# Optimization experiments

Measured on AMD Instinct MI355X. Metric: run time of the kernel, lower is better.

Reference implementation:

```python
import jax, jax.numpy as jnp
import numpy as np

N = 50000       # nodes
E = 800000      # edges (before self-loops)
G = 512         # graphs in batch
IN_DIM = 128
OUT_DIM = 8
DIMS = [(IN_DIM, 32), (32, 64), (64, 128), (128, 64)]
EPS = 1e-5


def setup_inputs() -> dict:
    key = jax.random.key(0)
    ks = jax.random.split(key, 40)
    def nrm(k, shape, s=0.05):
        return jax.random.normal(k, shape, jnp.float32) * s
    inp = {}
    inp["x"] = jax.random.normal(ks[0], (N, IN_DIM), jnp.float32)
    inp["edge_index"] = jax.random.randint(ks[1], (2, E), 0, N, dtype=jnp.int32)
    inp["batch"] = jnp.sort(jax.random.randint(ks[2], (N,), 0, G, dtype=jnp.int32))
    for i, (din, dout) in enumerate(DIMS, 1):
        inp[f"W{i}"]  = nrm(ks[3 * i + 0], (din, dout))
        inp[f"as{i}"] = nrm(ks[3 * i + 1], (dout,))
        inp[f"ad{i}"] = nrm(ks[3 * i + 2], (dout,))
        inp[f"b{i}"]  = jnp.zeros((dout,), jnp.float32)
        inp[f"g{i}"]  = jnp.ones((dout,), jnp.float32)   # BN gamma
        inp[f"be{i}"] = jnp.zeros((dout,), jnp.float32)  # BN beta
    inp["Wf"] = nrm(ks[20], (64, 32)); inp["bf"] = jnp.zeros((32,), jnp.float32)
    inp["Wc"] = nrm(ks[21], (32, OUT_DIM)); inp["bc"] = jnp.zeros((OUT_DIM,), jnp.float32)
    return inp


def gat_conv(x, src, dst, W, a_s, a_d, b):
    """PyG GATConv, heads=1: linear (no bias) -> per-edge attention with
    leaky_relu(0.2) -> segment softmax over incoming edges -> scatter-add -> bias."""
    h = x @ W                                   # [N, F]
    a_src = h @ a_s                             # [N]
    a_dst = h @ a_d                             # [N]
    e = jax.nn.leaky_relu(a_src[src] + a_dst[dst], 0.2)   # [E+N]
    m = jax.ops.segment_max(e, dst, num_segments=N)
    w = jnp.exp(e - m[dst])
    denom = jax.ops.segment_sum(w, dst, num_segments=N)
    alpha = w / denom[dst]                      # self-loops guarantee denom > 0
    out = jax.ops.segment_sum(alpha[:, None] * h[src], dst, num_segments=N)
    return out + b


def batch_norm(x, g, be):
    mu = x.mean(axis=0)
    var = x.var(axis=0)                         # biased, as torch training BN
    return (x - mu) * jax.lax.rsqrt(var + EPS) * g + be


def reference(x, edge_index, batch,
              W1, as1, ad1, b1, g1, be1,
              W2, as2, ad2, b2, g2, be2,
              W3, as3, ad3, b3, g3, be3,
              W4, as4, ad4, b4, g4, be4,
              Wf, bf, Wc, bc):
    loops = jnp.arange(N, dtype=edge_index.dtype)
    src = jnp.concatenate([edge_index[0], loops])   # GATConv adds self-loops
    dst = jnp.concatenate([edge_index[1], loops])
    params = [(W1, as1, ad1, b1, g1, be1), (W2, as2, ad2, b2, g2, be2),
              (W3, as3, ad3, b3, g3, be3), (W4, as4, ad4, b4, g4, be4)]
    h = x
    for (W, a_s, a_d, b, g, be) in params:
        h = jax.nn.leaky_relu(gat_conv(h, src, dst, W, a_s, a_d, b), 0.01)
        h = batch_norm(h, g, be)
    pooled = jax.ops.segment_sum(h, batch, num_segments=G)   # global_add_pool
    z = jax.nn.leaky_relu(pooled @ Wf + bf, 0.01)
    return jax.nn.sigmoid(z @ Wc + bc)
```

## Files before the change

### kernel.cpp

```cpp
#include <hip/hip_runtime.h>
#include <math.h>

constexpr int BLK = 256;
constexpr int NBLKA = 256;

static inline int cdiv(long a, long b) { return (int)((a + b - 1) / b); }

typedef __attribute__((ext_vector_type(8))) short short8;
typedef __attribute__((ext_vector_type(4))) float floatx4;

__device__ __forceinline__ unsigned short f2bf(float f) {
    unsigned u = __float_as_uint(f);
    unsigned r = u + 0x7fffu + ((u >> 16) & 1u);
    return (unsigned short)(r >> 16);
}
__device__ __forceinline__ float bf2f(unsigned short s) {
    return __uint_as_float(((unsigned)s) << 16);
}


__global__ void histA_k(const int* __restrict__ dst, int* __restrict__ histg,
                        int E, int nbkt, int chunk) {
    __shared__ int h[256];
    int tid = threadIdx.x, z = blockIdx.x;
    h[tid] = 0;
    __syncthreads();
    int e0 = z * chunk, e1 = min(E, e0 + chunk);
    for (int e = e0 + tid; e < e1; e += BLK) atomicAdd(&h[dst[e] >> 8], 1);
    __syncthreads();
    if (tid < nbkt) histg[z * nbkt + tid] = h[tid];
}

__global__ void bucket_scan_k(const int* __restrict__ histg, int* __restrict__ bucket_base,
                              int nbkt, int E, int* __restrict__ gs, int* __restrict__ ge,
                              int G, float* __restrict__ bnstats) {
    __shared__ int s[BLK];
    int t = threadIdx.x;
    int v = 0;
    if (t < nbkt)
        for (int z = 0; z < NBLKA; ++z) v += histg[z * nbkt + t];
    s[t] = v;
    __syncthreads();
    for (int o = 1; o < BLK; o <<= 1) {
        int tv = (t >= o) ? s[t - o] : 0;
        __syncthreads();
        s[t] += tv;
        __syncthreads();
    }
    if (t < nbkt) bucket_base[t] = s[t] - v;
    if (t == 0) bucket_base[nbkt] = E;
    for (int i = t; i < G; i += BLK) { gs[i] = 0x7fffffff; ge[i] = -1; }
    for (int i = t; i < 8192; i += BLK) bnstats[i] = 0.f;
}

__global__ void blk_scan_k(int* __restrict__ histg, const int* __restrict__ bucket_base,
                           int nbkt) {
    __shared__ int s[BLK];
    int t = threadIdx.x, b = blockIdx.x;
    int v = histg[t * nbkt + b];
    s[t] = v;
    __syncthreads();
    for (int o = 1; o < BLK; o <<= 1) {
        int tv = (t >= o) ? s[t - o] : 0;
        __syncthreads();
        s[t] += tv;
        __syncthreads();
    }
    histg[t * nbkt + b] = bucket_base[b] + s[t] - v;
}

__global__ void scatterA_k(const int* __restrict__ src, const int* __restrict__ dst,
                           const int* __restrict__ histg, unsigned* __restrict__ ebkt,
                           int E, int nbkt, int chunk) {
    __shared__ int cur[256];
    int tid = threadIdx.x, z = blockIdx.x;
    if (tid < nbkt) cur[tid] = histg[z * nbkt + tid];
    __syncthreads();
    int e0 = z * chunk, e1 = min(E, e0 + chunk);
    for (int e = e0 + tid; e < e1; e += BLK) {
        int d = dst[e];
        int b = d >> 8;
        int pos = atomicAdd(&cur[b], 1);
        ebkt[pos] = ((unsigned)(d & 255) << 16) | (unsigned)src[e];
    }
}

__global__ void csrB_k(const unsigned* __restrict__ ebkt, const int* __restrict__ bucket_base,
                       int* __restrict__ off, unsigned short* __restrict__ csr,
                       const int* __restrict__ batch, int* __restrict__ gs,
                       int* __restrict__ ge, int N, int E, int nbkt) {
    __shared__ int dg[256];
    __shared__ int sc[256];
    int t = threadIdx.x, b = blockIdx.x;
    int n0 = b << 8;
    int cnt = min(256, N - n0);
    dg[t] = (t < cnt) ? 1 : 0;
    __syncthreads();
    int e0 = bucket_base[b], e1 = bucket_base[b + 1];
    for (int e = e0 + t; e < e1; e += BLK) atomicAdd(&dg[ebkt[e] >> 16], 1);
    __syncthreads();
    int d = dg[t];
    sc[t] = d;
    __syncthreads();
    for (int o = 1; o < BLK; o <<= 1) {
        int tv = (t >= o) ? sc[t - o] : 0;
        __syncthreads();
        sc[t] += tv;
        __syncthreads();
    }
    int loff = sc[t] - d;
    int csrbase = e0 + n0;
    if (t < cnt) {
        off[n0 + t] = csrbase + loff;
        csr[csrbase + loff] = (unsigned short)(n0 + t);
        dg[t] = loff + 1;
    }
    if (b == nbkt - 1 && t == 0) off[N] = E + N;
    int n = n0 + t;
    if (n < N) {
        int bb = batch[n];
        if (n == 0) gs[bb] = 0;
        else {
            int pb = batch[n - 1];
            if (pb != bb) { gs[bb] = n; ge[pb] = n - 1; }
        }
        if (n == N - 1) ge[bb] = N - 1;
    }
    __syncthreads();
    for (int e = e0 + t; e < e1; e += BLK) {
        unsigned w = ebkt[e];
        int pos = atomicAdd(&dg[w >> 16], 1);
        csr[csrbase + pos] = (unsigned short)(w & 0xffff);
    }
}

template <int K, int NOUT, bool AFP32, bool HASBN>
__launch_bounds__(256)
__global__ void gemm_fused(const void* __restrict__ av, const float* __restrict__ W,
                           const float* __restrict__ a_s, const float* __restrict__ a_d,
                           const float* __restrict__ bnst, const float* __restrict__ g_prev,
                           const float* __restrict__ be_prev, float invN,
                           unsigned short* __restrict__ hb,
                           float* __restrict__ asrc, float* __restrict__ adst, int N) {
    constexpr int KF = K / 32;
    constexpr int NY = NOUT / 16;
    __shared__ float s_sca[K], s_scc[K], s_rs[K], s_rd[K], s_bd[2];
    int tid = threadIdx.x;
    if (tid < K) {
        float a = 1.f, c = 0.f;
        if (HASBN) {
            float su = 0.f, sq = 0.f;
#pragma unroll
            for (int s = 0; s < 8; ++s) {
                su += bnst[s * 256 + tid];
                sq += bnst[s * 256 + 128 + tid];
            }
            float mu = su * invN;
            float var = sq * invN - mu * mu;
            a = g_prev[tid] * rsqrtf(var + 1e-5f);
            c = be_prev[tid] - mu * a;
        }
        s_sca[tid] = a; s_scc[tid] = c;
    }
    __syncthreads();
    {
        if (tid < K) {
            const float* wr = W + (long)tid * NOUT;
            float rs = 0.f, rd = 0.f;
            for (int f = 0; f < NOUT; ++f) {
                float w = wr[f];
                rs += w * a_s[f];
                rd += w * a_d[f];
            }
            s_rs[tid] = rs; s_rd[tid] = rd;
        }
        __syncthreads();
        if (tid < 2) {
            const float* r = tid ? s_rd : s_rs;
            float b = 0.f;
            for (int k = 0; k < K; ++k) b += s_scc[k] * r[k];
            s_bd[tid] = b;
        }
        __syncthreads();
    }

    int wave = tid >> 6;
    int lane = tid & 63;
    int quad = lane >> 4;
    int r16 = lane & 15;
    int blockbase = blockIdx.x * 128;

    short8 afr[2][KF];
    bool valid[2];
#pragma unroll
    for (int rt = 0; rt < 2; ++rt) {
        int tilebase = blockbase + wave * 32 + rt * 16;
        valid[rt] = tilebase < N;
        if (!valid[rt]) continue;
        int arow = min(tilebase + r16, N - 1);
        if (AFP32) {
            const float* xr = (const float*)av + (long)arow * K;
#pragma unroll
            for (int kk = 0; kk < KF; ++kk) {
                float4 x0 = *(const float4*)(xr + kk * 32 + quad * 8);
                float4 x1 = *(const float4*)(xr + kk * 32 + quad * 8 + 4);
                short8 a;
                a[0] = (short)f2bf(x0.x); a[1] = (short)f2bf(x0.y);
                a[2] = (short)f2bf(x0.z); a[3] = (short)f2bf(x0.w);
                a[4] = (short)f2bf(x1.x); a[5] = (short)f2bf(x1.y);
                a[6] = (short)f2bf(x1.z); a[7] = (short)f2bf(x1.w);
                afr[rt][kk] = a;
            }
        } else {
            const unsigned short* hr = (const unsigned short*)av + (long)arow * K;
#pragma unroll
            for (int kk = 0; kk < KF; ++kk)
                afr[rt][kk] = *(const short8*)(hr + kk * 32 + quad * 8);
        }
        float ds = 0.f, dd = 0.f;
#pragma unroll
        for (int kk = 0; kk < KF; ++kk) {
            int kb = kk * 32 + quad * 8;
#pragma unroll
            for (int j = 0; j < 8; ++j) {
                int k = kb + j;
                float a = bf2f((unsigned short)afr[rt][kk][j]) * s_sca[k];
                ds += a * s_rs[k];
                dd += a * s_rd[k];
            }
        }
        ds += __shfl_xor(ds, 16, 64); ds += __shfl_xor(ds, 32, 64);
        dd += __shfl_xor(dd, 16, 64); dd += __shfl_xor(dd, 32, 64);
        int drow = tilebase + r16;
        if (quad == 0 && drow < N) {
            asrc[drow] = ds + s_bd[0];
            adst[drow] = dd + s_bd[1];
        }
    }

#pragma unroll
    for (int y = 0; y < NY; ++y) {
        int col = y * 16 + r16;
        short8 bfr[KF];
        float biasp = 0.f;
#pragma unroll
        for (int kk = 0; kk < KF; ++kk) {
            short8 b;
#pragma unroll
            for (int j = 0; j < 8; ++j) {
                int k = kk * 32 + quad * 8 + j;
                float w = W[(long)k * NOUT + col];
                b[j] = (short)f2bf(s_sca[k] * w);
                biasp += s_scc[k] * w;
            }
            bfr[kk] = b;
        }
        biasp += __shfl_xor(biasp, 16, 64);
        biasp += __shfl_xor(biasp, 32, 64);

#pragma unroll
        for (int rt = 0; rt < 2; ++rt) {
            if (!valid[rt]) continue;
            int tilebase = blockbase + wave * 32 + rt * 16;
            floatx4 acc = {0.f, 0.f, 0.f, 0.f};
#pragma unroll
            for (int kk = 0; kk < KF; ++kk)
                acc = __builtin_amdgcn_mfma_f32_16x16x32_bf16(afr[rt][kk], bfr[kk], acc, 0, 0, 0);
#pragma unroll
            for (int rr = 0; rr < 4; ++rr) {
                int srow = tilebase + quad * 4 + rr;
                if (srow < N) hb[(long)srow * NOUT + col] = f2bf(acc[rr] + biasp);
            }
        }
    }
}

template <int DOUT>
__global__ void gather_fused(const int* __restrict__ off,
                             const unsigned short* __restrict__ csr,
                             const float* __restrict__ asrc, const float* __restrict__ adst,
                             const unsigned short* __restrict__ hb,
                             const float* __restrict__ b,
                             unsigned short* __restrict__ out, int N) {
    constexpr int TPN = DOUT / 8;
    int t = blockIdx.x * blockDim.x + threadIdx.x;
    int d = t / TPN;
    if (d >= N) return;
    int l = t % TPN;
    int p0 = off[d], p1 = off[d + 1];
    float ad = adst[d];
    const int f0 = l * 8;

    float acc[8];
#pragma unroll
    for (int i = 0; i < 8; ++i) acc[i] = 0.f;
    float sum = 0.f;

#pragma unroll 2
    for (int p = p0; p < p1; ++p) {
        int s = csr[p];
        float e = asrc[s] + ad;
        e = e > 0.f ? e : 0.2f * e;
        float w = __expf(e);
        sum += w;
        const uint4 hv = *(const uint4*)(hb + (long)s * DOUT + f0);
        acc[0] += w * bf2f((unsigned short)(hv.x & 0xffff));
        acc[1] += w * bf2f((unsigned short)(hv.x >> 16));
        acc[2] += w * bf2f((unsigned short)(hv.y & 0xffff));
        acc[3] += w * bf2f((unsigned short)(hv.y >> 16));
        acc[4] += w * bf2f((unsigned short)(hv.z & 0xffff));
        acc[5] += w * bf2f((unsigned short)(hv.z >> 16));
        acc[6] += w * bf2f((unsigned short)(hv.w & 0xffff));
        acc[7] += w * bf2f((unsigned short)(hv.w >> 16));
    }
    float inv = 1.f / sum;

    float4 b0 = *(const float4*)(b + f0);
    float4 b1 = *(const float4*)(b + f0 + 4);
    float bb[8] = {b0.x, b0.y, b0.z, b0.w, b1.x, b1.y, b1.z, b1.w};
    ushort4 o0, o1;
#pragma unroll
    for (int i = 0; i < 8; ++i) {
        float v = acc[i] * inv + bb[i];
        v = v > 0.f ? v : 0.01f * v;
        unsigned short hv = f2bf(v);
        if (i < 4) ((unsigned short*)&o0)[i] = hv;
        else       ((unsigned short*)&o1)[i - 4] = hv;
    }
    *(ushort4*)(out + (long)d * DOUT + f0) = o0;
    *(ushort4*)(out + (long)d * DOUT + f0 + 4) = o1;
}

template <int DOUT>
__global__ void stats_k(const unsigned short* __restrict__ y, float* __restrict__ bn, int N) {
    constexpr int QPR = DOUT / 8;
    __shared__ float ssum[DOUT];
    __shared__ float ssq[DOUT];
    for (int i = threadIdx.x; i < DOUT; i += blockDim.x) { ssum[i] = 0.f; ssq[i] = 0.f; }
    __syncthreads();
    long total = (long)N * QPR;
    long stride = (long)gridDim.x * blockDim.x;
    long t0 = (long)blockIdx.x * blockDim.x + threadIdx.x;
    int f0 = (int)(t0 % QPR) * 8;
    float ls[8], lq[8];
#pragma unroll
    for (int i = 0; i < 8; ++i) { ls[i] = 0.f; lq[i] = 0.f; }
    for (long t = t0; t < total; t += stride) {
        uint4 hv = *(const uint4*)(y + t * 8);
        unsigned vv[4] = {hv.x, hv.y, hv.z, hv.w};
#pragma unroll
        for (int q = 0; q < 4; ++q) {
            float v0 = bf2f((unsigned short)(vv[q] & 0xffff));
            float v1 = bf2f((unsigned short)(vv[q] >> 16));
            ls[2 * q] += v0;     lq[2 * q] += v0 * v0;
            ls[2 * q + 1] += v1; lq[2 * q + 1] += v1 * v1;
        }
    }
#pragma unroll
    for (int i = 0; i < 8; ++i) {
        atomicAdd(&ssum[f0 + i], ls[i]);
        atomicAdd(&ssq[f0 + i], lq[i]);
    }
    __syncthreads();
    float* base = bn + (blockIdx.x & 7) * 256;
    for (int i = threadIdx.x; i < DOUT; i += blockDim.x) {
        atomicAdd(&base[i], ssum[i]);
        atomicAdd(&base[128 + i], ssq[i]);
    }
}

__global__ void pool_head_k(const unsigned short* __restrict__ h, const int* __restrict__ gs,
                            const int* __restrict__ ge, const float* __restrict__ bnst,
                            const float* __restrict__ g4, const float* __restrict__ be4,
                            float invN, const float* __restrict__ Wf,
                            const float* __restrict__ bf, const float* __restrict__ Wc,
                            const float* __restrict__ bc, float* __restrict__ out) {
    int g = blockIdx.x;
    int t = threadIdx.x;
    int f = t & 63, sub = t >> 6;
    __shared__ float pp[4][64];
    __shared__ float p[64];
    __shared__ float z[32];
    int s0 = gs[g], s1 = ge[g];
    float acc = 0.f;
    if (s0 <= s1)
        for (int n = s0 + sub; n <= s1; n += 4) acc += bf2f(h[(long)n * 64 + f]);
    pp[sub][f] = acc;
    __syncthreads();
    if (t < 64) {
        float su = 0.f, sq = 0.f;
#pragma unroll
        for (int s = 0; s < 8; ++s) {
            su += bnst[s * 256 + t];
            sq += bnst[s * 256 + 128 + t];
        }
        float mu = su * invN;
        float var = sq * invN - mu * mu;
        float a = g4[t] * rsqrtf(var + 1e-5f);
        float c = be4[t] - mu * a;
        float cnt = (s0 <= s1) ? (float)(s1 - s0 + 1) : 0.f;
        p[t] = a * (pp[0][t] + pp[1][t] + pp[2][t] + pp[3][t]) + cnt * c;
    }
    __syncthreads();
    if (t < 32) {
        float zacc = bf[t];
#pragma unroll
        for (int ff = 0; ff < 64; ++ff) zacc += p[ff] * Wf[ff * 32 + t];
        z[t] = zacc > 0.f ? zacc : 0.01f * zacc;
    }
    __syncthreads();
    if (t < 8) {
        float oacc = bc[t];
#pragma unroll
        for (int o = 0; o < 32; ++o) oacc += z[o] * Wc[o * 8 + t];
        out[(long)g * 8 + t] = 1.f / (1.f + __expf(-oacc));
    }
}

extern "C" void kernel_launch(void* const* d_in, const int* in_sizes, int n_in,
                              void* d_out, int out_size, void* d_ws, size_t ws_size,
                              hipStream_t stream) {
    const float* x   = (const float*)d_in[0];
    const int* ei    = (const int*)d_in[1];
    const int* batch = (const int*)d_in[2];
    const int N  = in_sizes[2];
    const int E  = in_sizes[1] / 2;
    const int ET = E + N;
    const int G  = out_size / 8;
    const int* src = ei;
    const int* dst = ei + E;

    const float *W[4], *as_[4], *ad_[4], *bb[4], *gg[4], *be_[4];
    for (int i = 0; i < 4; ++i) {
        W[i]   = (const float*)d_in[3 + 6 * i];
        as_[i] = (const float*)d_in[4 + 6 * i];
        ad_[i] = (const float*)d_in[5 + 6 * i];
        bb[i]  = (const float*)d_in[6 + 6 * i];
        gg[i]  = (const float*)d_in[7 + 6 * i];
        be_[i] = (const float*)d_in[8 + 6 * i];
    }
    const float* Wf = (const float*)d_in[27];
    const float* bfp = (const float*)d_in[28];
    const float* Wc = (const float*)d_in[29];
    const float* bc = (const float*)d_in[30];

    float* ws = (float*)d_ws;
    long off_ = 0;
    auto alloc = [&](long nelem) { float* p = ws + off_; off_ += (nelem + 3) & ~3L; return p; };
    unsigned short* h2a = (unsigned short*)alloc((long)N * 64);
    unsigned short* h2b = (unsigned short*)alloc((long)N * 64);
    unsigned short* hb  = (unsigned short*)alloc((long)N * 64);
    float* asrc     = alloc(N);
    float* adst     = alloc(N);
    float* bnstats  = alloc(4 * 2048);
    unsigned* ebkt  = (unsigned*)alloc(E);
    int* histg      = (int*)alloc((long)NBLKA * 256);
    int* bucket_base = (int*)alloc(260);
    int* off        = (int*)alloc(N + 1);
    unsigned short* csr = (unsigned short*)alloc(ET / 2 + 2);
    int* gs         = (int*)alloc(G);
    int* ge         = (int*)alloc(G);
    (void)ws_size; (void)n_in;

    const int nbkt = cdiv(N, 256);
    const int chunk = cdiv(E, NBLKA);
    const float invN = 1.f / (float)N;

    histA_k<<<NBLKA, BLK, 0, stream>>>(dst, histg, E, nbkt, chunk);
    bucket_scan_k<<<1, BLK, 0, stream>>>(histg, bucket_base, nbkt, E, gs, ge, G, bnstats);
    blk_scan_k<<<nbkt, BLK, 0, stream>>>(histg, bucket_base, nbkt);
    scatterA_k<<<NBLKA, BLK, 0, stream>>>(src, dst, histg, ebkt, E, nbkt, chunk);
    csrB_k<<<nbkt, BLK, 0, stream>>>(ebkt, bucket_base, off, csr, batch, gs, ge, N, E, nbkt);

#define LAYER(i, DIN, DOUT, AFP32, HASBN, INP, OUTP, BNPREV, GPREV, BEPREV)               \
    do {                                                                                  \
        gemm_fused<DIN, DOUT, AFP32, HASBN>                                               \
            <<<cdiv(N, 128), 256, 0, stream>>>(                                           \
                INP, W[i], as_[i], ad_[i], BNPREV, GPREV, BEPREV, invN,                   \
                hb, asrc, adst, N);                                                       \
        gather_fused<DOUT><<<cdiv((long)N * (DOUT / 8), BLK), BLK, 0, stream>>>(          \
            off, csr, asrc, adst, hb, bb[i], OUTP, N);                                    \
        stats_k<DOUT><<<240, BLK, 0, stream>>>(OUTP, bnstats + i * 2048, N);              \
    } while (0)

    LAYER(0, 128, 32, true, false, x, h2b, bnstats, gg[0], be_[0]);
    LAYER(1, 32, 64, false, true, h2b, h2a, bnstats + 0 * 2048, gg[0], be_[0]);
    LAYER(2, 64, 128, false, true, h2a, h2b, bnstats + 1 * 2048, gg[1], be_[1]);
    LAYER(3, 128, 64, false, true, h2b, h2a, bnstats + 2 * 2048, gg[2], be_[2]);
#undef LAYER

    pool_head_k<<<G, 256, 0, stream>>>(h2a, gs, ge, bnstats + 3 * 2048, gg[3], be_[3],
                                       invN, Wf, bfp, Wc, bc, (float*)d_out);
}
```

Baseline: 355.5 us.

## Restructure bucket scan and widen per-thread feature chunk in gather

Replaces the single-block serial bucket-total reduction with a per-bucket block scan that emits bucket sums, followed by a small scan to build bucket bases that scatterA adds on the fly. Separately, the gather kernel is templated on features per lane, so layers 2-4 process 16 features per thread instead of 8. This halves the redundant per-edge index, attention and exp work per node and packs the outputs with full 16-byte stores. The trade-off is fewer threads per node and more registers per thread.

```diff
diff --git a/kernel.cpp b/kernel.cpp
--- a/kernel.cpp
+++ b/kernel.cpp
@@ -31,14 +31,28 @@
     if (tid < nbkt) histg[z * nbkt + tid] = h[tid];
 }
 
-__global__ void bucket_scan_k(const int* __restrict__ histg, int* __restrict__ bucket_base,
-                              int nbkt, int E, int* __restrict__ gs, int* __restrict__ ge,
-                              int G, float* __restrict__ bnstats) {
+__global__ void blk_scan2_k(int* __restrict__ histg, int* __restrict__ bsum, int nbkt) {
+    __shared__ int s[BLK];
+    int t = threadIdx.x, b = blockIdx.x;
+    int v = histg[t * nbkt + b];
+    s[t] = v;
+    __syncthreads();
+    for (int o = 1; o < BLK; o <<= 1) {
+        int tv = (t >= o) ? s[t - o] : 0;
+        __syncthreads();
+        s[t] += tv;
+        __syncthreads();
+    }
+    histg[t * nbkt + b] = s[t] - v;
+    if (t == BLK - 1) bsum[b] = s[t];
+}
+
+__global__ void scan_base_k(const int* __restrict__ bsum, int* __restrict__ bucket_base,
+                            int nbkt, int E, int* __restrict__ gs, int* __restrict__ ge,
+                            int G, float* __restrict__ bnstats) {
     __shared__ int s[BLK];
     int t = threadIdx.x;
-    int v = 0;
-    if (t < nbkt)
-        for (int z = 0; z < NBLKA; ++z) v += histg[z * nbkt + t];
+    int v = (t < nbkt) ? bsum[t] : 0;
     s[t] = v;
     __syncthreads();
     for (int o = 1; o < BLK; o <<= 1) {
@@ -53,28 +67,12 @@
     for (int i = t; i < 8192; i += BLK) bnstats[i] = 0.f;
 }
 
-__global__ void blk_scan_k(int* __restrict__ histg, const int* __restrict__ bucket_base,
-                           int nbkt) {
-    __shared__ int s[BLK];
-    int t = threadIdx.x, b = blockIdx.x;
-    int v = histg[t * nbkt + b];
-    s[t] = v;
-    __syncthreads();
-    for (int o = 1; o < BLK; o <<= 1) {
-        int tv = (t >= o) ? s[t - o] : 0;
-        __syncthreads();
-        s[t] += tv;
-        __syncthreads();
-    }
-    histg[t * nbkt + b] = bucket_base[b] + s[t] - v;
-}
-
 __global__ void scatterA_k(const int* __restrict__ src, const int* __restrict__ dst,
-                           const int* __restrict__ histg, unsigned* __restrict__ ebkt,
-                           int E, int nbkt, int chunk) {
+                           const int* __restrict__ histg, const int* __restrict__ bucket_base,
+                           unsigned* __restrict__ ebkt, int E, int nbkt, int chunk) {
     __shared__ int cur[256];
     int tid = threadIdx.x, z = blockIdx.x;
-    if (tid < nbkt) cur[tid] = histg[z * nbkt + tid];
+    if (tid < nbkt) cur[tid] = histg[z * nbkt + tid] + bucket_base[tid];
     __syncthreads();
     int e0 = z * chunk, e1 = min(E, e0 + chunk);
     for (int e = e0 + tid; e < e1; e += BLK) {
@@ -275,25 +273,26 @@
     }
 }
 
-template <int DOUT>
+template <int DOUT, int FPL>
 __global__ void gather_fused(const int* __restrict__ off,
                              const unsigned short* __restrict__ csr,
                              const float* __restrict__ asrc, const float* __restrict__ adst,
                              const unsigned short* __restrict__ hb,
                              const float* __restrict__ b,
                              unsigned short* __restrict__ out, int N) {
-    constexpr int TPN = DOUT / 8;
+    constexpr int TPN = DOUT / FPL;
+    constexpr int NV = FPL / 8;
     int t = blockIdx.x * blockDim.x + threadIdx.x;
     int d = t / TPN;
     if (d >= N) return;
     int l = t % TPN;
     int p0 = off[d], p1 = off[d + 1];
     float ad = adst[d];
-    const int f0 = l * 8;
-
-    float acc[8];
-#pragma unroll
-    for (int i = 0; i < 8; ++i) acc[i] = 0.f;
+    const int f0 = l * FPL;
+
+    float acc[FPL];
+#pragma unroll
+    for (int i = 0; i < FPL; ++i) acc[i] = 0.f;
     float sum = 0.f;
 
 #pragma unroll 2
@@ -303,32 +302,38 @@
         e = e > 0.f ? e : 0.2f * e;
         float w = __expf(e);
         sum += w;
-        const uint4 hv = *(const uint4*)(hb + (long)s * DOUT + f0);
-        acc[0] += w * bf2f((unsigned short)(hv.x & 0xffff));
-        acc[1] += w * bf2f((unsigned short)(hv.x >> 16));
-        acc[2] += w * bf2f((unsigned short)(hv.y & 0xffff));
-        acc[3] += w * bf2f((unsigned short)(hv.y >> 16));
-        acc[4] += w * bf2f((unsigned short)(hv.z & 0xffff));
-        acc[5] += w * bf2f((unsigned short)(hv.z >> 16));
-        acc[6] += w * bf2f((unsigned short)(hv.w & 0xffff));
-        acc[7] += w * bf2f((unsigned short)(hv.w >> 16));
+        const unsigned short* hr = hb + (long)s * DOUT + f0;
+#pragma unroll
+        for (int v = 0; v < NV; ++v) {
+            const uint4 hv = *(const uint4*)(hr + v * 8);
+            acc[v * 8 + 0] += w * bf2f((unsigned short)(hv.x & 0xffff));
+            acc[v * 8 + 1] += w * bf2f((unsigned short)(hv.x >> 16));
+            acc[v * 8 + 2] += w * bf2f((unsigned short)(hv.y & 0xffff));
+            acc[v * 8 + 3] += w * bf2f((unsigned short)(hv.y >> 16));
+            acc[v * 8 + 4] += w * bf2f((unsigned short)(hv.z & 0xffff));
+            acc[v * 8 + 5] += w * bf2f((unsigned short)(hv.z >> 16));
+            acc[v * 8 + 6] += w * bf2f((unsigned short)(hv.w & 0xffff));
+            acc[v * 8 + 7] += w * bf2f((unsigned short)(hv.w >> 16));
+        }
     }
     float inv = 1.f / sum;
 
-    float4 b0 = *(const float4*)(b + f0);
-    float4 b1 = *(const float4*)(b + f0 + 4);
-    float bb[8] = {b0.x, b0.y, b0.z, b0.w, b1.x, b1.y, b1.z, b1.w};
-    ushort4 o0, o1;
-#pragma unroll
-    for (int i = 0; i < 8; ++i) {
-        float v = acc[i] * inv + bb[i];
-        v = v > 0.f ? v : 0.01f * v;
-        unsigned short hv = f2bf(v);
-        if (i < 4) ((unsigned short*)&o0)[i] = hv;
-        else       ((unsigned short*)&o1)[i - 4] = hv;
-    }
-    *(ushort4*)(out + (long)d * DOUT + f0) = o0;
-    *(ushort4*)(out + (long)d * DOUT + f0 + 4) = o1;
+#pragma unroll
+    for (int v = 0; v < NV; ++v) {
+        float4 b0 = *(const float4*)(b + f0 + v * 8);
+        float4 b1 = *(const float4*)(b + f0 + v * 8 + 4);
+        float bbv[8] = {b0.x, b0.y, b0.z, b0.w, b1.x, b1.y, b1.z, b1.w};
+        unsigned pk[4];
+#pragma unroll
+        for (int i = 0; i < 4; ++i) {
+            float v0 = acc[v * 8 + 2 * i] * inv + bbv[2 * i];
+            float v1 = acc[v * 8 + 2 * i + 1] * inv + bbv[2 * i + 1];
+            v0 = v0 > 0.f ? v0 : 0.01f * v0;
+            v1 = v1 > 0.f ? v1 : 0.01f * v1;
+            pk[i] = (unsigned)f2bf(v0) | ((unsigned)f2bf(v1) << 16);
+        }
+        *(uint4*)(out + (long)d * DOUT + f0 + v * 8) = uint4{pk[0], pk[1], pk[2], pk[3]};
+    }
 }
 
 template <int DOUT>
@@ -456,6 +461,7 @@
     unsigned* ebkt  = (unsigned*)alloc(E);
     int* histg      = (int*)alloc((long)NBLKA * 256);
     int* bucket_base = (int*)alloc(260);
+    int* bsum       = (int*)alloc(256);
     int* off        = (int*)alloc(N + 1);
     unsigned short* csr = (unsigned short*)alloc(ET / 2 + 2);
     int* gs         = (int*)alloc(G);
@@ -467,26 +473,26 @@
     const float invN = 1.f / (float)N;
 
     histA_k<<<NBLKA, BLK, 0, stream>>>(dst, histg, E, nbkt, chunk);
-    bucket_scan_k<<<1, BLK, 0, stream>>>(histg, bucket_base, nbkt, E, gs, ge, G, bnstats);
-    blk_scan_k<<<nbkt, BLK, 0, stream>>>(histg, bucket_base, nbkt);
-    scatterA_k<<<NBLKA, BLK, 0, stream>>>(src, dst, histg, ebkt, E, nbkt, chunk);
+    blk_scan2_k<<<nbkt, BLK, 0, stream>>>(histg, bsum, nbkt);
+    scan_base_k<<<1, BLK, 0, stream>>>(bsum, bucket_base, nbkt, E, gs, ge, G, bnstats);
+    scatterA_k<<<NBLKA, BLK, 0, stream>>>(src, dst, histg, bucket_base, ebkt, E, nbkt, chunk);
     csrB_k<<<nbkt, BLK, 0, stream>>>(ebkt, bucket_base, off, csr, batch, gs, ge, N, E, nbkt);
 
-#define LAYER(i, DIN, DOUT, AFP32, HASBN, INP, OUTP, BNPREV, GPREV, BEPREV)               \
+#define LAYER(i, DIN, DOUT, FPL, AFP32, HASBN, INP, OUTP, BNPREV, GPREV, BEPREV)          \
     do {                                                                                  \
         gemm_fused<DIN, DOUT, AFP32, HASBN>                                               \
             <<<cdiv(N, 128), 256, 0, stream>>>(                                           \
                 INP, W[i], as_[i], ad_[i], BNPREV, GPREV, BEPREV, invN,                   \
                 hb, asrc, adst, N);                                                       \
-        gather_fused<DOUT><<<cdiv((long)N * (DOUT / 8), BLK), BLK, 0, stream>>>(          \
+        gather_fused<DOUT, FPL><<<cdiv((long)N * (DOUT / FPL), BLK), BLK, 0, stream>>>(   \
             off, csr, asrc, adst, hb, bb[i], OUTP, N);                                    \
         stats_k<DOUT><<<240, BLK, 0, stream>>>(OUTP, bnstats + i * 2048, N);              \
     } while (0)
 
-    LAYER(0, 128, 32, true, false, x, h2b, bnstats, gg[0], be_[0]);
-    LAYER(1, 32, 64, false, true, h2b, h2a, bnstats + 0 * 2048, gg[0], be_[0]);
-    LAYER(2, 64, 128, false, true, h2a, h2b, bnstats + 1 * 2048, gg[1], be_[1]);
-    LAYER(3, 128, 64, false, true, h2b, h2a, bnstats + 2 * 2048, gg[2], be_[2]);
+    LAYER(0, 128, 32, 8,  true,  false, x,   h2b, bnstats,            gg[0], be_[0]);
+    LAYER(1, 32,  64, 16, false, true,  h2b, h2a, bnstats + 0 * 2048, gg[0], be_[0]);
+    LAYER(2, 64, 128, 16, false, true,  h2a, h2b, bnstats + 1 * 2048, gg[1], be_[1]);
+    LAYER(3, 128, 64, 16, false, true,  h2b, h2a, bnstats + 2 * 2048, gg[2], be_[2]);
 #undef LAYER
 
     pool_head_k<<<G, 256, 0, stream>>>(h2a, gs, ge, bnstats + 3 * 2048, gg[3], be_[3],
```

After: 353.2 us. No clear change (-0.6%).
